# Performance work log

Hardware: AMD Instinct MI355X
Metric: run time of the kernel (lower is better)

Reference implementation:

```python
import jax, jax.numpy as jnp
import numpy as np
import math

TAU_MEM = 20.0
ALPHA = math.exp(-1.0 / TAU_MEM)
BASE_THRESHOLD = 1.0


def setup_inputs() -> dict:
    key = jax.random.key(0)
    k1, k2, k3 = jax.random.split(key, 3)
    B, T, D, H = 32, 1024, 512, 512
    x = jax.random.normal(k1, (B, T, D), dtype=jnp.float32)
    # nn.Linear default init: U(-1/sqrt(D), 1/sqrt(D))
    bound = 1.0 / math.sqrt(D)
    W = jax.random.uniform(k2, (H, D), dtype=jnp.float32, minval=-bound, maxval=bound)
    b = jax.random.uniform(k3, (H,), dtype=jnp.float32, minval=-bound, maxval=bound)
    threshold_adapt = jnp.ones((H,), dtype=jnp.float32) * BASE_THRESHOLD
    return {"x": x, "W": W, "b": b, "threshold_adapt": threshold_adapt}


def reference(x, W, b, threshold_adapt):
    B, T, D = x.shape
    H = W.shape[0]
    # One batched GEMM instead of T small ones (same math as fc(x[:, t]) per step)
    xlin = jnp.einsum('btd,hd->bth', x, W) + b  # [B, T, H]
    xlin_t = jnp.transpose(xlin, (1, 0, 2))     # [T, B, H]

    def step(mem, xt):
        mem = ALPHA * mem + xt
        # torch std: unbiased (ddof=1), over hidden dim; B>1 branch
        mem_std = jnp.std(mem, axis=-1, keepdims=True, ddof=1)  # [B, 1]
        thr = threshold_adapt[None, :] + 0.1 * mem_std           # [B, H]
        spike = (mem >= thr).astype(mem.dtype)
        mem = mem * (1.0 - spike)
        return mem, spike

    mem0 = jnp.zeros((B, H), dtype=x.dtype)
    mem, spikes_t = jax.lax.scan(step, mem0, xlin_t)
    spikes = jnp.transpose(spikes_t, (1, 0, 2))  # [B, T, H]
    return spikes, mem
```

## Files before the change

### kernel.cpp

```cpp
#include <hip/hip_runtime.h>


#define ALPHA_F 0.95122942450071402f

constexpr int Bb = 32, T = 1024, D = 512, Hh = 512;
constexpr int M = Bb * T;
constexpr int NBLOCKS = 512;
constexpr int NTILES = (M / 128) * (Hh / 128);
constexpr int SIG_PER_CHUNK = 4;

#define BM 128
#define BK 16

template <int CTRL>
__device__ __forceinline__ float dpp_add(float v) {
  int s = __builtin_amdgcn_update_dpp(0, __builtin_bit_cast(int, v),
                                      CTRL, 0xF, 0xF, true);
  return v + __builtin_bit_cast(float, s);
}

__device__ __forceinline__ float dpp_reduce(float v) {
  v = dpp_add<0x111>(v);
  v = dpp_add<0x112>(v);
  v = dpp_add<0x114>(v);
  v = dpp_add<0x118>(v);
  v = dpp_add<0x142>(v);
  v = dpp_add<0x143>(v);
  return v;
}

__global__ void zero_ws_kernel(unsigned* ws) {
  if (threadIdx.x < 257) ws[threadIdx.x] = 0;
}

__global__ __launch_bounds__(256) void fused_kernel(
    const float* __restrict__ X,
    const float* __restrict__ W,
    const float* __restrict__ bias,
    const float* __restrict__ ta,
    float* out,
    float* memout,
    unsigned* ws)
{
  unsigned* prog = ws;
  unsigned* ticket = ws + 256;
  const int tid = threadIdx.x;
  const int bid = (int)blockIdx.x;

  if (bid >= 256 && bid < 288) return;

  if (bid >= 32) {
    __shared__ float As[BK][BM + 4];
    __shared__ float Bs[BK][BM + 4];
    __shared__ unsigned s_g;
    const int tm = tid >> 4;
    const int tn = tid & 15;

    for (;;) {
      __syncthreads();
      if (tid == 0)
        s_g = __hip_atomic_fetch_add(ticket, 1u, __ATOMIC_RELAXED,
                                     __HIP_MEMORY_SCOPE_AGENT);
      __syncthreads();
      const unsigned g = s_g;
      if (g >= (unsigned)NTILES) break;
      const int ch  = (int)(g >> 7);
      const int idx = (int)(g & 127u);
      const int b   = idx >> 2;
      const int bn  = idx & 3;
      const int bmt = b * 8 + ch;
      const int rowA = bmt * BM;
      const int rowB = bn * BM;

      float acc[8][8];
#pragma unroll
      for (int i = 0; i < 8; ++i)
#pragma unroll
        for (int j = 0; j < 8; ++j) acc[i][j] = 0.f;

      for (int k0 = 0; k0 < D; k0 += BK) {
        __syncthreads();
#pragma unroll
        for (int i = 0; i < 2; ++i) {
          const int f = tid * 2 + i;
          const int r = f >> 2;
          const int c4 = (f & 3) << 2;
          float4 a = *(const float4*)(X + (size_t)(rowA + r) * D + k0 + c4);
          As[c4 + 0][r] = a.x; As[c4 + 1][r] = a.y;
          As[c4 + 2][r] = a.z; As[c4 + 3][r] = a.w;
          float4 w = *(const float4*)(W + (size_t)(rowB + r) * D + k0 + c4);
          Bs[c4 + 0][r] = w.x; Bs[c4 + 1][r] = w.y;
          Bs[c4 + 2][r] = w.z; Bs[c4 + 3][r] = w.w;
        }
        __syncthreads();
#pragma unroll
        for (int k = 0; k < BK; ++k) {
          float4 a0 = *(const float4*)&As[k][tm * 4];
          float4 a1 = *(const float4*)&As[k][64 + tm * 4];
          float4 b0 = *(const float4*)&Bs[k][tn * 4];
          float4 b1 = *(const float4*)&Bs[k][64 + tn * 4];
          float av[8] = {a0.x, a0.y, a0.z, a0.w, a1.x, a1.y, a1.z, a1.w};
          float bv[8] = {b0.x, b0.y, b0.z, b0.w, b1.x, b1.y, b1.z, b1.w};
#pragma unroll
          for (int i = 0; i < 8; ++i)
#pragma unroll
            for (int j = 0; j < 8; ++j)
              acc[i][j] = fmaf(av[i], bv[j], acc[i][j]);
        }
      }

      const int c0 = rowB + tn * 4;
      const int c1 = rowB + 64 + tn * 4;
      float4 bb0 = *(const float4*)(bias + c0);
      float4 bb1 = *(const float4*)(bias + c1);
      float bc[8] = {bb0.x, bb0.y, bb0.z, bb0.w, bb1.x, bb1.y, bb1.z, bb1.w};
#pragma unroll
      for (int i = 0; i < 8; ++i) {
        const int r = rowA + ((i < 4) ? (tm * 4 + i) : (64 + tm * 4 + (i - 4)));
        float4 v0, v1;
        v0.x = acc[i][0] + bc[0]; v0.y = acc[i][1] + bc[1];
        v0.z = acc[i][2] + bc[2]; v0.w = acc[i][3] + bc[3];
        v1.x = acc[i][4] + bc[4]; v1.y = acc[i][5] + bc[5];
        v1.z = acc[i][6] + bc[6]; v1.w = acc[i][7] + bc[7];
        *(float4*)(out + (size_t)r * Hh + c0) = v0;
        *(float4*)(out + (size_t)r * Hh + c1) = v1;
      }
      __syncthreads();
      if (tid == 0)
        __hip_atomic_fetch_add(prog + bmt, 1u, __ATOMIC_RELEASE,
                               __HIP_MEMORY_SCOPE_AGENT);
    }
    return;
  }

  if (tid >= 64) return;
  __builtin_amdgcn_s_setprio(3);

  const int b = bid;
  const int lane = tid;
  float* base = out + (size_t)b * (size_t)(T * Hh);
  const int h0 = lane * 4;
  const int h1 = 256 + lane * 4;

  float4 tav0 = *(const float4*)(ta + h0);
  float4 tav1 = *(const float4*)(ta + h1);
  float tac[8] = {tav0.x, tav0.y, tav0.z, tav0.w,
                  tav1.x, tav1.y, tav1.z, tav1.w};

#define WAIT_CHUNK(idxc)                                                     \
  {                                                                          \
    unsigned* wp = prog + (idxc);                                            \
    while (__hip_atomic_load(wp, __ATOMIC_RELAXED,                           \
                             __HIP_MEMORY_SCOPE_AGENT) <                     \
           (unsigned)SIG_PER_CHUNK) {                                        \
      __builtin_amdgcn_s_sleep(2);                                           \
    }                                                                        \
    __builtin_amdgcn_fence(__ATOMIC_ACQUIRE, "agent");                       \
  }

  float4 pA0[8], pB0[8], pA1[8], pB1[8];
  float cc[8], mr[8];
  bool fire[8];
#pragma unroll
  for (int i = 0; i < 8; ++i) fire[i] = false;

#define LOAD1(NA, NB, u, t)                                                  \
  NA[u] = *(const float4*)(base + (size_t)(t) * Hh + h0);                    \
  NB[u] = *(const float4*)(base + (size_t)(t) * Hh + h1);

#define STEPX(CA, CB, u, t, NXA, NXB, SPEC)                                  \
  {                                                                          \
    const float xu_[8] = {CA[u].x, CA[u].y, CA[u].z, CA[u].w,                \
                          CB[u].x, CB[u].y, CB[u].z, CB[u].w};               \
    _Pragma("unroll")                                                        \
    for (int i = 0; i < 8; ++i) mr[i] = fire[i] ? xu_[i] : cc[i];            \
    float s_ = ((mr[0] + mr[1]) + (mr[2] + mr[3])) +                         \
               ((mr[4] + mr[5]) + (mr[6] + mr[7]));                          \
    float q_ = ((fmaf(mr[0], mr[0], mr[1] * mr[1])) +                        \
                (fmaf(mr[2], mr[2], mr[3] * mr[3]))) +                       \
               ((fmaf(mr[4], mr[4], mr[5] * mr[5])) +                        \
                (fmaf(mr[6], mr[6], mr[7] * mr[7])));                        \
    if (SPEC) {           \
      const float4 nxa_ = (NXA), nxb_ = (NXB);                               \
      const float xn_[8] = {nxa_.x, nxa_.y, nxa_.z, nxa_.w,                  \
                            nxb_.x, nxb_.y, nxb_.z, nxb_.w};                 \
      _Pragma("unroll")                                                      \
      for (int i = 0; i < 8; ++i) cc[i] = fmaf(ALPHA_F, mr[i], xn_[i]);      \
    }                                                                        \
    s_ = dpp_reduce(s_);                                                     \
    q_ = dpp_reduce(q_);                                                     \
    float var_ = fmaf(s_ * s_, -(1.0f / Hh), q_) * (1.0f / (Hh - 1));        \
    var_ = fmaxf(var_, 0.f);                                                 \
    float sdl_ = __builtin_amdgcn_sqrtf(var_);            \
    const float sd_ = __builtin_bit_cast(                                    \
        float,                                                               \
        __builtin_amdgcn_readlane(__builtin_bit_cast(int, sdl_), 63));       \
    float sp_[8];                                                            \
    _Pragma("unroll")                                                        \
    for (int i = 0; i < 8; ++i) {                                            \
      fire[i] = mr[i] >= fmaf(0.1f, sd_, tac[i]);                            \
      sp_[i] = fire[i] ? 1.f : 0.f;                                          \
    }                                                                        \
    *(float4*)(base + (size_t)(t) * Hh + h0) =                               \
        make_float4(sp_[0], sp_[1], sp_[2], sp_[3]);                         \
    *(float4*)(base + (size_t)(t) * Hh + h1) =                               \
        make_float4(sp_[4], sp_[5], sp_[6], sp_[7]);                         \
  }

#define GROUP(CA, CB, NA, NB, T0, PF, LASTG)                                 \
  {                                                                          \
    if (PF) {                                                                \
      LOAD1(NA, NB, 0, (T0) + 8)  LOAD1(NA, NB, 1, (T0) + 9)                 \
      LOAD1(NA, NB, 2, (T0) + 10) LOAD1(NA, NB, 3, (T0) + 11)                \
      LOAD1(NA, NB, 4, (T0) + 12) LOAD1(NA, NB, 5, (T0) + 13)                \
      LOAD1(NA, NB, 6, (T0) + 14) LOAD1(NA, NB, 7, (T0) + 15)                \
    }                                                                        \
    STEPX(CA, CB, 0, (T0) + 0, CA[1], CB[1], 1)                              \
    STEPX(CA, CB, 1, (T0) + 1, CA[2], CB[2], 1)                              \
    STEPX(CA, CB, 2, (T0) + 2, CA[3], CB[3], 1)                              \
    STEPX(CA, CB, 3, (T0) + 3, CA[4], CB[4], 1)                              \
    STEPX(CA, CB, 4, (T0) + 4, CA[5], CB[5], 1)                              \
    STEPX(CA, CB, 5, (T0) + 5, CA[6], CB[6], 1)                              \
    STEPX(CA, CB, 6, (T0) + 6, CA[7], CB[7], 1)                              \
    STEPX(CA, CB, 7, (T0) + 7, NA[0], NB[0], !(LASTG))                       \
  }

  WAIT_CHUNK(b * 8);
  LOAD1(pA0, pB0, 0, 0) LOAD1(pA0, pB0, 1, 1)
  LOAD1(pA0, pB0, 2, 2) LOAD1(pA0, pB0, 3, 3)
  LOAD1(pA0, pB0, 4, 4) LOAD1(pA0, pB0, 5, 5)
  LOAD1(pA0, pB0, 6, 6) LOAD1(pA0, pB0, 7, 7)
  cc[0] = pA0[0].x; cc[1] = pA0[0].y; cc[2] = pA0[0].z; cc[3] = pA0[0].w;
  cc[4] = pB0[0].x; cc[5] = pB0[0].y; cc[6] = pB0[0].z; cc[7] = pB0[0].w;

  for (int gp = 0; gp < 63; ++gp) {
    const int t0 = gp << 4;
    GROUP(pA0, pB0, pA1, pB1, t0, true, false)
    if ((gp & 7) == 7) WAIT_CHUNK(b * 8 + ((t0 + 16) >> 7));
    GROUP(pA1, pB1, pA0, pB0, t0 + 8, true, false)
  }
  GROUP(pA0, pB0, pA1, pB1, 1008, true, false)
  GROUP(pA1, pB1, pA0, pB0, 1016, false, true)

#undef GROUP
#undef STEPX
#undef LOAD1
#undef WAIT_CHUNK

  float mf[8];
#pragma unroll
  for (int i = 0; i < 8; ++i) mf[i] = fire[i] ? 0.f : mr[i];
  *(float4*)(memout + (size_t)b * Hh + h0) = make_float4(mf[0], mf[1], mf[2], mf[3]);
  *(float4*)(memout + (size_t)b * Hh + h1) = make_float4(mf[4], mf[5], mf[6], mf[7]);
}

__global__ __launch_bounds__(256) void gemm_kernel(
    const float* __restrict__ X, const float* __restrict__ W,
    const float* __restrict__ bias, float* __restrict__ out) {
  const int bn = blockIdx.x, bm = blockIdx.y;
  __shared__ float As[BK][BM + 4];
  __shared__ float Bs[BK][BM + 4];
  const int tid = threadIdx.x, tm = tid >> 4, tn = tid & 15;
  float acc[8][8];
#pragma unroll
  for (int i = 0; i < 8; ++i)
#pragma unroll
    for (int j = 0; j < 8; ++j) acc[i][j] = 0.f;
  const int rowA = bm * BM, rowB = bn * BM;
  for (int k0 = 0; k0 < D; k0 += BK) {
    __syncthreads();
#pragma unroll
    for (int i = 0; i < 2; ++i) {
      const int f = tid * 2 + i, r = f >> 2, c4 = (f & 3) << 2;
      float4 a = *(const float4*)(X + (size_t)(rowA + r) * D + k0 + c4);
      As[c4 + 0][r] = a.x; As[c4 + 1][r] = a.y;
      As[c4 + 2][r] = a.z; As[c4 + 3][r] = a.w;
      float4 w = *(const float4*)(W + (size_t)(rowB + r) * D + k0 + c4);
      Bs[c4 + 0][r] = w.x; Bs[c4 + 1][r] = w.y;
      Bs[c4 + 2][r] = w.z; Bs[c4 + 3][r] = w.w;
    }
    __syncthreads();
#pragma unroll
    for (int k = 0; k < BK; ++k) {
      float4 a0 = *(const float4*)&As[k][tm * 4];
      float4 a1 = *(const float4*)&As[k][64 + tm * 4];
      float4 b0 = *(const float4*)&Bs[k][tn * 4];
      float4 b1 = *(const float4*)&Bs[k][64 + tn * 4];
      float av[8] = {a0.x, a0.y, a0.z, a0.w, a1.x, a1.y, a1.z, a1.w};
      float bv[8] = {b0.x, b0.y, b0.z, b0.w, b1.x, b1.y, b1.z, b1.w};
#pragma unroll
      for (int i = 0; i < 8; ++i)
#pragma unroll
        for (int j = 0; j < 8; ++j)
          acc[i][j] = fmaf(av[i], bv[j], acc[i][j]);
    }
  }
  const int c0 = rowB + tn * 4, c1 = rowB + 64 + tn * 4;
  float4 bb0 = *(const float4*)(bias + c0);
  float4 bb1 = *(const float4*)(bias + c1);
  float bc[8] = {bb0.x, bb0.y, bb0.z, bb0.w, bb1.x, bb1.y, bb1.z, bb1.w};
#pragma unroll
  for (int i = 0; i < 8; ++i) {
    const int r = rowA + ((i < 4) ? (tm * 4 + i) : (64 + tm * 4 + (i - 4)));
    float4 v0, v1;
    v0.x = acc[i][0] + bc[0]; v0.y = acc[i][1] + bc[1];
    v0.z = acc[i][2] + bc[2]; v0.w = acc[i][3] + bc[3];
    v1.x = acc[i][4] + bc[4]; v1.y = acc[i][5] + bc[5];
    v1.z = acc[i][6] + bc[6]; v1.w = acc[i][7] + bc[7];
    *(float4*)(out + (size_t)r * Hh + c0) = v0;
    *(float4*)(out + (size_t)r * Hh + c1) = v1;
  }
}

__global__ __launch_bounds__(64) void scan_kernel(
    float* __restrict__ xs, const float* __restrict__ ta,
    float* __restrict__ memout) {
  const int b = blockIdx.x, lane = threadIdx.x;
  float* base = xs + (size_t)b * (size_t)(T * Hh);
  const int h0 = lane * 4, h1 = 256 + lane * 4;
  float4 tav0 = *(const float4*)(ta + h0);
  float4 tav1 = *(const float4*)(ta + h1);
  float tac[8] = {tav0.x, tav0.y, tav0.z, tav0.w,
                  tav1.x, tav1.y, tav1.z, tav1.w};
  float4 pa[4], pb[4];
#pragma unroll
  for (int u = 0; u < 4; ++u) {
    pa[u] = *(const float4*)(base + (size_t)u * Hh + h0);
    pb[u] = *(const float4*)(base + (size_t)u * Hh + h1);
  }
  float xc[8], cc[8], mr[8];
  bool fire[8];
  {
    const float4 a = pa[0], bq = pb[0];
    xc[0] = a.x; xc[1] = a.y; xc[2] = a.z; xc[3] = a.w;
    xc[4] = bq.x; xc[5] = bq.y; xc[6] = bq.z; xc[7] = bq.w;
  }
#pragma unroll
  for (int i = 0; i < 8; ++i) { cc[i] = xc[i]; fire[i] = false; }
#pragma unroll 4
  for (int t = 0; t < T; ++t) {
    const int u = t & 3;
    if (t + 4 < T) {
      pa[u] = *(const float4*)(base + (size_t)(t + 4) * Hh + h0);
      pb[u] = *(const float4*)(base + (size_t)(t + 4) * Hh + h1);
    }
#pragma unroll
    for (int i = 0; i < 8; ++i) mr[i] = fire[i] ? xc[i] : cc[i];
    float s = ((mr[0] + mr[1]) + (mr[2] + mr[3])) +
              ((mr[4] + mr[5]) + (mr[6] + mr[7]));
    float q = ((mr[0] * mr[0] + mr[1] * mr[1]) +
               (mr[2] * mr[2] + mr[3] * mr[3])) +
              ((mr[4] * mr[4] + mr[5] * mr[5]) +
               (mr[6] * mr[6] + mr[7] * mr[7]));
    {
      const float4 na = pa[(u + 1) & 3];
      const float4 nb = pb[(u + 1) & 3];
      xc[0] = na.x; xc[1] = na.y; xc[2] = na.z; xc[3] = na.w;
      xc[4] = nb.x; xc[5] = nb.y; xc[6] = nb.z; xc[7] = nb.w;
#pragma unroll
      for (int i = 0; i < 8; ++i) cc[i] = fmaf(ALPHA_F, mr[i], xc[i]);
    }
    s = dpp_reduce(s);
    q = dpp_reduce(q);
    float var = fmaxf((q - s * s * (1.0f / Hh)) * (1.0f / (Hh - 1)), 0.f);
    float sdl = __builtin_amdgcn_sqrtf(var);
    const float sd = __builtin_bit_cast(
        float, __builtin_amdgcn_readlane(__builtin_bit_cast(int, sdl), 63));
    float sp[8];
#pragma unroll
    for (int i = 0; i < 8; ++i) {
      fire[i] = mr[i] >= fmaf(0.1f, sd, tac[i]);
      sp[i] = fire[i] ? 1.f : 0.f;
    }
    *(float4*)(base + (size_t)t * Hh + h0) = make_float4(sp[0], sp[1], sp[2], sp[3]);
    *(float4*)(base + (size_t)t * Hh + h1) = make_float4(sp[4], sp[5], sp[6], sp[7]);
  }
  float mf[8];
#pragma unroll
  for (int i = 0; i < 8; ++i) mf[i] = fire[i] ? 0.f : mr[i];
  *(float4*)(memout + (size_t)b * Hh + h0) = make_float4(mf[0], mf[1], mf[2], mf[3]);
  *(float4*)(memout + (size_t)b * Hh + h1) = make_float4(mf[4], mf[5], mf[6], mf[7]);
}

extern "C" void kernel_launch(void* const* d_in, const int* in_sizes, int n_in,
                              void* d_out, int out_size, void* d_ws,
                              size_t ws_size, hipStream_t stream) {
  const float* x    = (const float*)d_in[0];
  const float* W    = (const float*)d_in[1];
  const float* bias = (const float*)d_in[2];
  const float* ta   = (const float*)d_in[3];

  float* out    = (float*)d_out;
  float* spikes = out;
  float* memout = out + (size_t)Bb * T * Hh;

  if (ws_size >= 257 * sizeof(unsigned)) {
    unsigned* ws = (unsigned*)d_ws;
    zero_ws_kernel<<<dim3(1), dim3(512), 0, stream>>>(ws);
    fused_kernel<<<dim3(NBLOCKS), dim3(256), 0, stream>>>(
        x, W, bias, ta, spikes, memout, ws);
  } else {
    dim3 ggrid(Hh / 128, M / BM);
    gemm_kernel<<<ggrid, dim3(256), 0, stream>>>(x, W, bias, spikes);
    scan_kernel<<<dim3(Bb), dim3(64), 0, stream>>>(spikes, ta, memout);
  }
}
```

Measured before the change: 318.0 us.

## Split recurrent scan across two wavefronts with LDS exchange of partial sums

The sequential spiking scan per batch row used to run on one wavefront handling 8 hidden units per lane. It now uses two wavefronts, each owning half the hidden dimension with 4 units per lane. Each wave reduces its partial sum and sum of squares with DPP, then swaps the partials through double-buffered shared memory guarded by a sequence-number spin flag. This halves the per-step ALU and load work on the serial critical path, at the cost of a cross-wave handshake through LDS on every timestep.

```diff
diff --git a/kernel.cpp b/kernel.cpp
--- a/kernel.cpp
+++ b/kernel.cpp
@@ -27,6 +27,11 @@
   v = dpp_add<0x142>(v);
   v = dpp_add<0x143>(v);
   return v;
+}
+
+__device__ __forceinline__ float rd63(float v) {
+  return __builtin_bit_cast(
+      float, __builtin_amdgcn_readlane(__builtin_bit_cast(int, v), 63));
 }
 
 __global__ void zero_ws_kernel(unsigned* ws) {
@@ -133,19 +138,21 @@
     return;
   }
 
-  if (tid >= 64) return;
+  __shared__ __align__(8) float2 xch[2][2];
+  __shared__ unsigned xseq[2][2];
+  if (tid < 4) xseq[tid >> 1][tid & 1] = 0u;
+  __syncthreads();
+  if (tid >= 128) return;
   __builtin_amdgcn_s_setprio(3);
 
   const int b = bid;
-  const int lane = tid;
+  const int w = tid >> 6;
+  const int lane = tid & 63;
   float* base = out + (size_t)b * (size_t)(T * Hh);
-  const int h0 = lane * 4;
-  const int h1 = 256 + lane * 4;
-
-  float4 tav0 = *(const float4*)(ta + h0);
-  float4 tav1 = *(const float4*)(ta + h1);
-  float tac[8] = {tav0.x, tav0.y, tav0.z, tav0.w,
-                  tav1.x, tav1.y, tav1.z, tav1.w};
+  const int h0 = w * 256 + lane * 4;
+
+  float4 tav = *(const float4*)(ta + h0);
+  float tac[4] = {tav.x, tav.y, tav.z, tav.w};
 
 #define WAIT_CHUNK(idxc)                                                     \
   {                                                                          \
@@ -158,100 +165,99 @@
     __builtin_amdgcn_fence(__ATOMIC_ACQUIRE, "agent");                       \
   }
 
-  float4 pA0[8], pB0[8], pA1[8], pB1[8];
-  float cc[8], mr[8];
-  bool fire[8];
-#pragma unroll
-  for (int i = 0; i < 8; ++i) fire[i] = false;
-
-#define LOAD1(NA, NB, u, t)                                                  \
-  NA[u] = *(const float4*)(base + (size_t)(t) * Hh + h0);                    \
-  NB[u] = *(const float4*)(base + (size_t)(t) * Hh + h1);
-
-#define STEPX(CA, CB, u, t, NXA, NXB, SPEC)                                  \
+  float4 pA0[8], pA1[8];
+  float cc[4], mr[4];
+  bool fire[4];
+#pragma unroll
+  for (int i = 0; i < 4; ++i) fire[i] = false;
+
+#define LOAD1(NA, u, t)                                                      \
+  NA[u] = *(const float4*)(base + (size_t)(t) * Hh + h0);
+
+#define STEPX(CA, u, t, NX, SPEC)                                            \
   {                                                                          \
-    const float xu_[8] = {CA[u].x, CA[u].y, CA[u].z, CA[u].w,                \
-                          CB[u].x, CB[u].y, CB[u].z, CB[u].w};               \
+    const float xu_[4] = {CA[u].x, CA[u].y, CA[u].z, CA[u].w};               \
     _Pragma("unroll")                                                        \
-    for (int i = 0; i < 8; ++i) mr[i] = fire[i] ? xu_[i] : cc[i];            \
-    float s_ = ((mr[0] + mr[1]) + (mr[2] + mr[3])) +                         \
-               ((mr[4] + mr[5]) + (mr[6] + mr[7]));                          \
-    float q_ = ((fmaf(mr[0], mr[0], mr[1] * mr[1])) +                        \
-                (fmaf(mr[2], mr[2], mr[3] * mr[3]))) +                       \
-               ((fmaf(mr[4], mr[4], mr[5] * mr[5])) +                        \
-                (fmaf(mr[6], mr[6], mr[7] * mr[7])));                        \
+    for (int i = 0; i < 4; ++i) mr[i] = fire[i] ? xu_[i] : cc[i];            \
+    float s_ = (mr[0] + mr[1]) + (mr[2] + mr[3]);                            \
+    float q_ = fmaf(mr[0], mr[0], mr[1] * mr[1]) +                           \
+               fmaf(mr[2], mr[2], mr[3] * mr[3]);                            \
     if (SPEC) {           \
-      const float4 nxa_ = (NXA), nxb_ = (NXB);                               \
-      const float xn_[8] = {nxa_.x, nxa_.y, nxa_.z, nxa_.w,                  \
-                            nxb_.x, nxb_.y, nxb_.z, nxb_.w};                 \
-      _Pragma("unroll")                                                      \
-      for (int i = 0; i < 8; ++i) cc[i] = fmaf(ALPHA_F, mr[i], xn_[i]);      \
+      const float4 nx_ = (NX);                                               \
+      cc[0] = fmaf(ALPHA_F, mr[0], nx_.x);                                   \
+      cc[1] = fmaf(ALPHA_F, mr[1], nx_.y);                                   \
+      cc[2] = fmaf(ALPHA_F, mr[2], nx_.z);                                   \
+      cc[3] = fmaf(ALPHA_F, mr[3], nx_.w);                                   \
     }                                                                        \
     s_ = dpp_reduce(s_);                                                     \
     q_ = dpp_reduce(q_);                                                     \
-    float var_ = fmaf(s_ * s_, -(1.0f / Hh), q_) * (1.0f / (Hh - 1));        \
+    const int sl_ = (t) & 1;                                                 \
+    if (lane == 63) {                                                        \
+      xch[sl_][w] = make_float2(s_, q_);                                     \
+      __hip_atomic_store(&xseq[sl_][w], (unsigned)((t) + 1),                 \
+                         __ATOMIC_RELEASE, __HIP_MEMORY_SCOPE_WORKGROUP);    \
+    }                                                                        \
+    while (__hip_atomic_load(&xseq[sl_][w ^ 1], __ATOMIC_ACQUIRE,            \
+                             __HIP_MEMORY_SCOPE_WORKGROUP) <                 \
+           (unsigned)((t) + 1)) {}                                           \
+    const float2 o_ = xch[sl_][w ^ 1];                                       \
+    const float sm_ = rd63(s_) + o_.x;    \
+    const float qm_ = rd63(q_) + o_.y;                                       \
+    float var_ = fmaf(sm_ * sm_, -(1.0f / Hh), qm_) * (1.0f / (Hh - 1));     \
     var_ = fmaxf(var_, 0.f);                                                 \
-    float sdl_ = __builtin_amdgcn_sqrtf(var_);            \
-    const float sd_ = __builtin_bit_cast(                                    \
-        float,                                                               \
-        __builtin_amdgcn_readlane(__builtin_bit_cast(int, sdl_), 63));       \
-    float sp_[8];                                                            \
+    const float sd_ = __builtin_amdgcn_sqrtf(var_);   \
+    float sp_[4];                                                            \
     _Pragma("unroll")                                                        \
-    for (int i = 0; i < 8; ++i) {                                            \
+    for (int i = 0; i < 4; ++i) {                                            \
       fire[i] = mr[i] >= fmaf(0.1f, sd_, tac[i]);                            \
       sp_[i] = fire[i] ? 1.f : 0.f;                                          \
     }                                                                        \
     *(float4*)(base + (size_t)(t) * Hh + h0) =                               \
         make_float4(sp_[0], sp_[1], sp_[2], sp_[3]);                         \
-    *(float4*)(base + (size_t)(t) * Hh + h1) =                               \
-        make_float4(sp_[4], sp_[5], sp_[6], sp_[7]);                         \
-  }
-
-#define GROUP(CA, CB, NA, NB, T0, PF, LASTG)                                 \
+  }
+
+#define GROUP(CA, NA, T0, PF, LASTG)                                         \
   {                                                                          \
     if (PF) {                                                                \
-      LOAD1(NA, NB, 0, (T0) + 8)  LOAD1(NA, NB, 1, (T0) + 9)                 \
-      LOAD1(NA, NB, 2, (T0) + 10) LOAD1(NA, NB, 3, (T0) + 11)                \
-      LOAD1(NA, NB, 4, (T0) + 12) LOAD1(NA, NB, 5, (T0) + 13)                \
-      LOAD1(NA, NB, 6, (T0) + 14) LOAD1(NA, NB, 7, (T0) + 15)                \
+      LOAD1(NA, 0, (T0) + 8)  LOAD1(NA, 1, (T0) + 9)                         \
+      LOAD1(NA, 2, (T0) + 10) LOAD1(NA, 3, (T0) + 11)                        \
+      LOAD1(NA, 4, (T0) + 12) LOAD1(NA, 5, (T0) + 13)                        \
+      LOAD1(NA, 6, (T0) + 14) LOAD1(NA, 7, (T0) + 15)                        \
     }                                                                        \
-    STEPX(CA, CB, 0, (T0) + 0, CA[1], CB[1], 1)                              \
-    STEPX(CA, CB, 1, (T0) + 1, CA[2], CB[2], 1)                              \
-    STEPX(CA, CB, 2, (T0) + 2, CA[3], CB[3], 1)                              \
-    STEPX(CA, CB, 3, (T0) + 3, CA[4], CB[4], 1)                              \
-    STEPX(CA, CB, 4, (T0) + 4, CA[5], CB[5], 1)                              \
-    STEPX(CA, CB, 5, (T0) + 5, CA[6], CB[6], 1)                              \
-    STEPX(CA, CB, 6, (T0) + 6, CA[7], CB[7], 1)                              \
-    STEPX(CA, CB, 7, (T0) + 7, NA[0], NB[0], !(LASTG))                       \
+    STEPX(CA, 0, (T0) + 0, CA[1], 1)                                         \
+    STEPX(CA, 1, (T0) + 1, CA[2], 1)                                         \
+    STEPX(CA, 2, (T0) + 2, CA[3], 1)                                         \
+    STEPX(CA, 3, (T0) + 3, CA[4], 1)                                         \
+    STEPX(CA, 4, (T0) + 4, CA[5], 1)                                         \
+    STEPX(CA, 5, (T0) + 5, CA[6], 1)                                         \
+    STEPX(CA, 6, (T0) + 6, CA[7], 1)                                         \
+    STEPX(CA, 7, (T0) + 7, NA[0], !(LASTG))                                  \
   }
 
   WAIT_CHUNK(b * 8);
-  LOAD1(pA0, pB0, 0, 0) LOAD1(pA0, pB0, 1, 1)
-  LOAD1(pA0, pB0, 2, 2) LOAD1(pA0, pB0, 3, 3)
-  LOAD1(pA0, pB0, 4, 4) LOAD1(pA0, pB0, 5, 5)
-  LOAD1(pA0, pB0, 6, 6) LOAD1(pA0, pB0, 7, 7)
+  LOAD1(pA0, 0, 0) LOAD1(pA0, 1, 1) LOAD1(pA0, 2, 2) LOAD1(pA0, 3, 3)
+  LOAD1(pA0, 4, 4) LOAD1(pA0, 5, 5) LOAD1(pA0, 6, 6) LOAD1(pA0, 7, 7)
   cc[0] = pA0[0].x; cc[1] = pA0[0].y; cc[2] = pA0[0].z; cc[3] = pA0[0].w;
-  cc[4] = pB0[0].x; cc[5] = pB0[0].y; cc[6] = pB0[0].z; cc[7] = pB0[0].w;
 
   for (int gp = 0; gp < 63; ++gp) {
     const int t0 = gp << 4;
-    GROUP(pA0, pB0, pA1, pB1, t0, true, false)
+    GROUP(pA0, pA1, t0, true, false)
     if ((gp & 7) == 7) WAIT_CHUNK(b * 8 + ((t0 + 16) >> 7));
-    GROUP(pA1, pB1, pA0, pB0, t0 + 8, true, false)
-  }
-  GROUP(pA0, pB0, pA1, pB1, 1008, true, false)
-  GROUP(pA1, pB1, pA0, pB0, 1016, false, true)
+    GROUP(pA1, pA0, t0 + 8, true, false)
+  }
+  GROUP(pA0, pA1, 1008, true, false)
+  GROUP(pA1, pA0, 1016, false, true)
 
 #undef GROUP
 #undef STEPX
 #undef LOAD1
 #undef WAIT_CHUNK
 
-  float mf[8];
-#pragma unroll
-  for (int i = 0; i < 8; ++i) mf[i] = fire[i] ? 0.f : mr[i];
-  *(float4*)(memout + (size_t)b * Hh + h0) = make_float4(mf[0], mf[1], mf[2], mf[3]);
-  *(float4*)(memout + (size_t)b * Hh + h1) = make_float4(mf[4], mf[5], mf[6], mf[7]);
+  float mf[4];
+#pragma unroll
+  for (int i = 0; i < 4; ++i) mf[i] = fire[i] ? 0.f : mr[i];
+  *(float4*)(memout + (size_t)b * Hh + h0) =
+      make_float4(mf[0], mf[1], mf[2], mf[3]);
 }
 
 __global__ __launch_bounds__(256) void gemm_kernel(
@@ -364,8 +370,7 @@
     q = dpp_reduce(q);
     float var = fmaxf((q - s * s * (1.0f / Hh)) * (1.0f / (Hh - 1)), 0.f);
     float sdl = __builtin_amdgcn_sqrtf(var);
-    const float sd = __builtin_bit_cast(
-        float, __builtin_amdgcn_readlane(__builtin_bit_cast(int, sdl), 63));
+    const float sd = rd63(sdl);
     float sp[8];
 #pragma unroll
     for (int i = 0; i < 8; ++i) {
```

Result: slower. 430.1 us (+35.3%).
